# Performance work log

Hardware: AMD Instinct MI355X
Metric: run time of the kernel (lower is better)

The kernel has to match this reference:

```python
import jax, jax.numpy as jnp
import numpy as np

B, S, D = 2, 2048, 1024
H, DH = 16, 64
WINDOW = 256


def setup_inputs() -> dict:
    key = jax.random.key(0)
    ks = jax.random.split(key, 11)
    s = 1.0 / np.sqrt(D)
    return {
        "query": jax.random.normal(ks[0], (B, S, D), jnp.float32),
        "key": jax.random.normal(ks[1], (B, S, D), jnp.float32),
        "value": jax.random.normal(ks[2], (B, S, D), jnp.float32),
        "Wq": jax.random.normal(ks[3], (D, D), jnp.float32) * s,
        "bq": jax.random.normal(ks[4], (D,), jnp.float32) * s,
        "Wk": jax.random.normal(ks[5], (D, D), jnp.float32) * s,
        "bk": jax.random.normal(ks[6], (D,), jnp.float32) * s,
        "Wv": jax.random.normal(ks[7], (D, D), jnp.float32) * s,
        "bv": jax.random.normal(ks[8], (D,), jnp.float32) * s,
        "Wo": jax.random.normal(ks[9], (D, D), jnp.float32) * s,
        "bo": jax.random.normal(ks[10], (D,), jnp.float32) * s,
    }


def reference(query, key, value, Wq, bq, Wk, bk, Wv, bv, Wo, bo):
    scale = DH ** -0.5
    # projections (torch Linear: x @ W.T + b)
    q = query @ Wq.T + bq  # [B,S,D]
    k = key @ Wk.T + bk
    v = value @ Wv.T + bv
    # split heads -> [B,H,S,DH]
    q = q.reshape(B, S, H, DH).transpose(0, 2, 1, 3)
    k = k.reshape(B, S, H, DH).transpose(0, 2, 1, 3)
    v = v.reshape(B, S, H, DH).transpose(0, 2, 1, 3)
    # dense scores with sliding-window causal mask
    attn = jnp.einsum('bhqd,bhkd->bhqk', q, k) * scale  # [B,H,S,S]
    q_idx = jnp.arange(S)[:, None]
    k_idx = jnp.arange(S)[None, :]
    keep = (k_idx <= q_idx) & (k_idx >= q_idx - WINDOW + 1)  # causal & window
    attn = jnp.where(keep[None, None], attn, -jnp.inf)
    attn = jax.nn.softmax(attn, axis=-1)
    # dropout_p=0.0 (eval) -> identity
    out = jnp.einsum('bhqk,bhkd->bhqd', attn, v)  # [B,H,S,DH]
    out = out.transpose(0, 2, 1, 3).reshape(B, S, D)
    return out @ Wo.T + bo
```

## Files before the change

kernel.cpp:

```cpp
#include <hip/hip_runtime.h>
#include <cstdint>
#include <cstddef>

#define B_   2
#define S_   2048
#define D_   1024
#define H_   16
#define DH_  64
#define NROW (B_ * S_)

typedef __bf16  bf16x8 __attribute__((ext_vector_type(8)));
typedef __bf16  bf16x4 __attribute__((ext_vector_type(4)));
typedef float   f32x4  __attribute__((ext_vector_type(4)));

#define MFMA16(a, b, c) __builtin_amdgcn_mfma_f32_16x16x32_bf16((a), (b), (c), 0, 0, 0)

__device__ __forceinline__ void gload_lds16(const void* g, void* l) {
  __builtin_amdgcn_global_load_lds(
      (__attribute__((address_space(1))) void*)(g),
      (__attribute__((address_space(3))) void*)(l), 16, 0, 0);
}

struct CastArgs { const float* src[7]; __bf16* dst[7]; };

__global__ void cast_all(CastArgs a) {
  int b = blockIdx.x, which, idx;
  if (b < 12288) { which = b >> 12; idx = b & 4095; }
  else { b -= 12288; which = 3 + (b >> 10); idx = b & 1023; }
  const int i = idx * 256 + threadIdx.x;
  const float4 v = ((const float4*)a.src[which])[i];
  bf16x4 o;
  o[0] = (__bf16)v.x; o[1] = (__bf16)v.y; o[2] = (__bf16)v.z; o[3] = (__bf16)v.w;
  ((bf16x4*)a.dst[which])[i] = o;
}

struct QKVArgs {
  const __bf16* A[3]; const __bf16* W[3]; const float* bias[3]; __bf16* C[3];
};

__global__ __launch_bounds__(256, 2) void gemm_qkv(QKVArgs args) {
  __shared__ __bf16 As[128 * 32];
  __shared__ __bf16 Bs[128 * 32];
  const int z = blockIdx.z;
  const __bf16* A = args.A[z];
  const __bf16* W = args.W[z];
  const float* bias = args.bias[z];
  __bf16* C = args.C[z];
  const int tid  = threadIdx.x;
  const int lane = tid & 63, wave = tid >> 6;
  const int lo   = lane & 15, quad = lane >> 4;
  const int wr   = wave & 1,  wc   = wave >> 1;
  const int bn   = blockIdx.x, bm = blockIdx.y;
  const __bf16* Ag = A + (size_t)bn * 128 * D_;
  const __bf16* Wg = W + (size_t)bm * 128 * D_;
  const int c0 = tid, c1 = tid + 256;
  const int r0 = c0 >> 2, s0 = (c0 & 3) * 8;
  const int r1 = c1 >> 2, s1 = (c1 & 3) * 8;

  f32x4 acc[4][4] = {};
  for (int k0 = 0; k0 < D_; k0 += 32) {
    __syncthreads();
    gload_lds16(Ag + (size_t)r0 * D_ + k0 + s0, &As[c0 * 8]);
    gload_lds16(Ag + (size_t)r1 * D_ + k0 + s1, &As[c1 * 8]);
    gload_lds16(Wg + (size_t)r0 * D_ + k0 + s0, &Bs[c0 * 8]);
    gload_lds16(Wg + (size_t)r1 * D_ + k0 + s1, &Bs[c1 * 8]);
    __syncthreads();
    bf16x8 af[4], bfr[4];
#pragma unroll
    for (int i = 0; i < 4; i++)
      af[i] = *(const bf16x8*)&As[(wr * 64 + i * 16 + lo) * 32 + quad * 8];
#pragma unroll
    for (int j = 0; j < 4; j++)
      bfr[j] = *(const bf16x8*)&Bs[(wc * 64 + j * 16 + lo) * 32 + quad * 8];
#pragma unroll
    for (int i = 0; i < 4; i++)
#pragma unroll
      for (int j = 0; j < 4; j++)
        acc[i][j] = MFMA16(af[i], bfr[j], acc[i][j]);
  }
  if (z == 2) {
#pragma unroll
    for (int i = 0; i < 4; i++) {
      const int row0 = bn * 128 + wr * 64 + i * 16 + quad * 4;
      const int bb = row0 >> 11, s = row0 & (S_ - 1);
#pragma unroll
      for (int j = 0; j < 4; j++) {
        const int col = bm * 128 + wc * 64 + j * 16 + lo;
        const int hh = col >> 6, dd = col & 63;
        const float bv = bias[col];
        bf16x4 o;
#pragma unroll
        for (int r = 0; r < 4; r++) o[r] = (__bf16)(acc[i][j][r] + bv);
        *(bf16x4*)&C[((size_t)(bb * H_ + hh) * DH_ + dd) * S_ + s] = o;
      }
    }
  } else {
#pragma unroll
    for (int i = 0; i < 4; i++) {
      const int row = bn * 128 + wr * 64 + i * 16 + quad * 4;
#pragma unroll
      for (int j = 0; j < 4; j++) {
        const int col = bm * 128 + wc * 64 + j * 16 + lo;
        const float bv = bias[col];
#pragma unroll
        for (int r = 0; r < 4; r++)
          C[(size_t)(row + r) * D_ + col] = (__bf16)(acc[i][j][r] + bv);
      }
    }
  }
}

__global__ __launch_bounds__(256, 2) void attn_win4(
    const __bf16* __restrict__ Qp, const __bf16* __restrict__ Kp,
    const __bf16* __restrict__ Vt, __bf16* __restrict__ ctx) {
  __shared__ __bf16 smem[20992];
  const int qt = blockIdx.x, h = blockIdx.y, b = blockIdx.z;
  const int q0 = qt * 64;
  const int tid = threadIdx.x, wave = tid >> 6, lane = tid & 63;
  const int lo = lane & 15, quad = lane >> 4;
  const int tmin = (q0 >= 256) ? 0 : ((256 - q0) >> 6);
  const __bf16* Kg = Kp + (size_t)b * S_ * D_ + h * DH_;
  const __bf16* Vg = Vt + (size_t)(b * H_ + h) * DH_ * S_;
  const size_t qbase = ((size_t)b * S_) * D_ + h * DH_;

  const int c0 = tid, c1 = tid + 256;
  const int rA = c0 >> 3, gA = ((c0 & 7) ^ (rA & 7)) * 8;
  const int rB = c1 >> 3, gB = ((c1 & 7) ^ (rB & 7)) * 8;

  auto stageK = [&](int t) {
    const int k0 = q0 - 256 + t * 64;
    const int kb = (t & 1) * 4096;
    gload_lds16(Kg + (size_t)(k0 + rA) * D_ + gA, &smem[kb + c0 * 8]);
    gload_lds16(Kg + (size_t)(k0 + rB) * D_ + gB, &smem[kb + c1 * 8]);
  };
  auto stageV = [&](int t) {
    const int k0 = q0 - 256 + t * 64;
    const int vb = 8192 + (t & 1) * 4096;
    gload_lds16(Vg + (size_t)rA * S_ + k0 + gA, &smem[vb + c0 * 8]);
    gload_lds16(Vg + (size_t)rB * S_ + k0 + gB, &smem[vb + c1 * 8]);
  };

  const int qrow = q0 + wave * 16 + lo;
  const bf16x8 qf0 = *(const bf16x8*)&Qp[qbase + (size_t)qrow * D_ + quad * 8];
  const bf16x8 qf1 = *(const bf16x8*)&Qp[qbase + (size_t)qrow * D_ + 32 + quad * 8];

  stageK(tmin); stageV(tmin);
  if (tmin + 1 <= 4) { stageK(tmin + 1); stageV(tmin + 1); }
  __syncthreads();

  const int g0 = (quad ^ (lo & 7)) * 8;
  const int g1 = ((quad + 4) ^ (lo & 7)) * 8;

  const float scale = 0.125f;
  const int dbase = lo - wave * 16 - quad * 4 - 256;
  const int pw = 16384 + wave * 1152;

  float m_[4] = {-3e38f, -3e38f, -3e38f, -3e38f};
  float l_[4] = {0.f, 0.f, 0.f, 0.f};
  f32x4 oacc[4] = {};

#pragma unroll
  for (int t = 0; t < 5; t++) {
    if (t < tmin) continue;
    const int kb = (t & 1) * 4096, vb = 8192 + (t & 1) * 4096;
    f32x4 sc[4];
#pragma unroll
    for (int kt = 0; kt < 4; kt++) {
      const int kr = kt * 16 + lo;
      const bf16x8 kf0 = *(const bf16x8*)&smem[kb + kr * 64 + g0];
      const bf16x8 kf1 = *(const bf16x8*)&smem[kb + kr * 64 + g1];
      f32x4 c = {0.f, 0.f, 0.f, 0.f};
      c = MFMA16(qf0, kf0, c);
      c = MFMA16(qf1, kf1, c);
      sc[kt] = c;
    }
    float tmax[4] = {-3e38f, -3e38f, -3e38f, -3e38f};
#pragma unroll
    for (int kt = 0; kt < 4; kt++)
#pragma unroll
      for (int r = 0; r < 4; r++) {
        const int delta = dbase + t * 64 + kt * 16 - r;
        const bool keep = (delta <= 0) && (delta > -256);
        const float v = keep ? sc[kt][r] * scale : -3e38f;
        sc[kt][r] = v;
        tmax[r] = fmaxf(tmax[r], v);
      }
#pragma unroll
    for (int r = 0; r < 4; r++)
#pragma unroll
      for (int off = 1; off < 16; off <<= 1)
        tmax[r] = fmaxf(tmax[r], __shfl_xor(tmax[r], off));
    float alpha[4];
#pragma unroll
    for (int r = 0; r < 4; r++) {
      const float mn = fmaxf(m_[r], tmax[r]);
      alpha[r] = __expf(m_[r] - mn);
      m_[r] = mn;
    }
    float rs[4] = {0.f, 0.f, 0.f, 0.f};
#pragma unroll
    for (int kt = 0; kt < 4; kt++)
#pragma unroll
      for (int r = 0; r < 4; r++) {
        const float p = __expf(sc[kt][r] - m_[r]);
        sc[kt][r] = p;
        rs[r] += p;
      }
#pragma unroll
    for (int r = 0; r < 4; r++) {
#pragma unroll
      for (int off = 1; off < 16; off <<= 1)
        rs[r] += __shfl_xor(rs[r], off);
      l_[r] = l_[r] * alpha[r] + rs[r];
    }
#pragma unroll
    for (int ds = 0; ds < 4; ds++)
#pragma unroll
      for (int r = 0; r < 4; r++)
        oacc[ds][r] *= alpha[r];
#pragma unroll
    for (int kt = 0; kt < 4; kt++)
#pragma unroll
      for (int r = 0; r < 4; r++)
        smem[pw + (quad * 4 + r) * 72 + kt * 16 + lo] = (__bf16)sc[kt][r];
    const bf16x8 pf0 = *(const bf16x8*)&smem[pw + lo * 72 + quad * 8];
    const bf16x8 pf1 = *(const bf16x8*)&smem[pw + lo * 72 + 32 + quad * 8];
#pragma unroll
    for (int ds = 0; ds < 4; ds++) {
      const bf16x8 vf0 = *(const bf16x8*)&smem[vb + (ds * 16 + lo) * 64 + g0];
      const bf16x8 vf1 = *(const bf16x8*)&smem[vb + (ds * 16 + lo) * 64 + g1];
      oacc[ds] = MFMA16(pf0, vf0, oacc[ds]);
      oacc[ds] = MFMA16(pf1, vf1, oacc[ds]);
    }
    if (t < 4) {
      __syncthreads();
      if (t + 2 <= 4) { stageK(t + 2); stageV(t + 2); }
    }
  }

#pragma unroll
  for (int ds = 0; ds < 4; ds++)
#pragma unroll
    for (int r = 0; r < 4; r++) {
      const int qg = q0 + wave * 16 + quad * 4 + r;
      ctx[((size_t)b * S_ + qg) * D_ + h * DH_ + ds * 16 + lo] =
          (__bf16)(oacc[ds][r] / l_[r]);
    }
}

__global__ __launch_bounds__(256, 2) void gemm_o(
    const __bf16* __restrict__ A, const __bf16* __restrict__ W,
    const float* __restrict__ bias, float* __restrict__ C) {
  __shared__ __bf16 As[64 * 32];
  __shared__ __bf16 Bs[128 * 32];
  const int tid = threadIdx.x, lane = tid & 63, wave = tid >> 6;
  const int lo = lane & 15, quad = lane >> 4;
  const int wr = wave & 1, wc = wave >> 1;
  const int bn = blockIdx.x, bm = blockIdx.y;
  const __bf16* Ag = A + (size_t)bn * 64 * D_;
  const __bf16* Wg = W + (size_t)bm * 128 * D_;
  const int ra = tid >> 2, sa = (tid & 3) * 8;
  const int cb0 = tid, cb1 = tid + 256;
  const int rb0 = cb0 >> 2, sb0 = (cb0 & 3) * 8;
  const int rb1 = cb1 >> 2, sb1 = (cb1 & 3) * 8;
  f32x4 acc[2][4] = {};
  for (int k0 = 0; k0 < D_; k0 += 32) {
    __syncthreads();
    gload_lds16(Ag + (size_t)ra * D_ + k0 + sa, &As[tid * 8]);
    gload_lds16(Wg + (size_t)rb0 * D_ + k0 + sb0, &Bs[cb0 * 8]);
    gload_lds16(Wg + (size_t)rb1 * D_ + k0 + sb1, &Bs[cb1 * 8]);
    __syncthreads();
    bf16x8 af[2], bfr[4];
#pragma unroll
    for (int i = 0; i < 2; i++)
      af[i] = *(const bf16x8*)&As[(wr * 32 + i * 16 + lo) * 32 + quad * 8];
#pragma unroll
    for (int j = 0; j < 4; j++)
      bfr[j] = *(const bf16x8*)&Bs[(wc * 64 + j * 16 + lo) * 32 + quad * 8];
#pragma unroll
    for (int i = 0; i < 2; i++)
#pragma unroll
      for (int j = 0; j < 4; j++)
        acc[i][j] = MFMA16(af[i], bfr[j], acc[i][j]);
  }
#pragma unroll
  for (int i = 0; i < 2; i++) {
    const int row = bn * 64 + wr * 32 + i * 16 + quad * 4;
#pragma unroll
    for (int j = 0; j < 4; j++) {
      const int col = bm * 128 + wc * 64 + j * 16 + lo;
      const float bv = bias[col];
#pragma unroll
      for (int r = 0; r < 4; r++)
        C[(size_t)(row + r) * D_ + col] = acc[i][j][r] + bv;
    }
  }
}

extern "C" void kernel_launch(void* const* d_in, const int* in_sizes, int n_in,
                              void* d_out, int out_size, void* d_ws, size_t ws_size,
                              hipStream_t stream) {
  (void)in_sizes; (void)n_in; (void)out_size; (void)ws_size;
  const float* q_in = (const float*)d_in[0];
  const float* k_in = (const float*)d_in[1];
  const float* v_in = (const float*)d_in[2];
  const float* Wq   = (const float*)d_in[3];
  const float* bq   = (const float*)d_in[4];
  const float* Wk   = (const float*)d_in[5];
  const float* bk   = (const float*)d_in[6];
  const float* Wv   = (const float*)d_in[7];
  const float* bv   = (const float*)d_in[8];
  const float* Wo   = (const float*)d_in[9];
  const float* bo   = (const float*)d_in[10];

  const size_t XN = (size_t)NROW * D_;
  const size_t WN = (size_t)D_ * D_;
  char* ws = (char*)d_ws;
  __bf16* xq  = (__bf16*)ws; ws += XN * 2;
  __bf16* xk  = (__bf16*)ws; ws += XN * 2;
  __bf16* xv  = (__bf16*)ws; ws += XN * 2;
  __bf16* wqb = (__bf16*)ws; ws += WN * 2;
  __bf16* wkb = (__bf16*)ws; ws += WN * 2;
  __bf16* wvb = (__bf16*)ws; ws += WN * 2;
  __bf16* wob = (__bf16*)ws; ws += WN * 2;
  __bf16* Qp  = (__bf16*)ws; ws += XN * 2;
  __bf16* Kp  = (__bf16*)ws; ws += XN * 2;
  __bf16* Vtp = (__bf16*)ws; ws += XN * 2;
  __bf16* ctx = (__bf16*)ws; ws += XN * 2;

  CastArgs ca;
  ca.src[0] = q_in; ca.src[1] = k_in; ca.src[2] = v_in;
  ca.src[3] = Wq; ca.src[4] = Wk; ca.src[5] = Wv; ca.src[6] = Wo;
  ca.dst[0] = xq; ca.dst[1] = xk; ca.dst[2] = xv;
  ca.dst[3] = wqb; ca.dst[4] = wkb; ca.dst[5] = wvb; ca.dst[6] = wob;
  cast_all<<<16384, 256, 0, stream>>>(ca);

  QKVArgs qa;
  qa.A[0] = xq;  qa.A[1] = xk;  qa.A[2] = xv;
  qa.W[0] = wqb; qa.W[1] = wkb; qa.W[2] = wvb;
  qa.bias[0] = bq; qa.bias[1] = bk; qa.bias[2] = bv;
  qa.C[0] = Qp; qa.C[1] = Kp; qa.C[2] = Vtp;
  gemm_qkv<<<dim3(NROW / 128, D_ / 128, 3), 256, 0, stream>>>(qa);

  attn_win4<<<dim3(S_ / 64, H_, B_), 256, 0, stream>>>(Qp, Kp, Vtp, ctx);

  gemm_o<<<dim3(NROW / 64, D_ / 128), 256, 0, stream>>>(ctx, wob, bo, (float*)d_out);
}
```

Measured before the change: 197.4 us.

## Widen attention query tile to 128 and drop online-softmax max tracking

The sliding-window attention kernel now gives each block 128 query rows, with 32 rows per wave. Each K/V tile staged in LDS is therefore reused across twice as many queries, and the grid is halved. Waves skip K tiles that fall entirely outside their window. The running max, rescale and per-tile shuffle reductions are replaced by a fixed exponent offset, exp(s*scale - 8), and the row sums are reduced once at the end. This saves ALU and shuffle work, but it loses the overflow and underflow protection for large score magnitudes, and the larger LDS footprint with occupancy 3 may limit residency.

Measured after the change: 194.9 us. Within noise of the previous version (-1.3%).

```diff
diff --git a/kernel.cpp b/kernel.cpp
--- a/kernel.cpp
+++ b/kernel.cpp
@@ -110,12 +110,12 @@
   }
 }
 
-__global__ __launch_bounds__(256, 2) void attn_win4(
+__global__ __launch_bounds__(256, 3) void attn_win5(
     const __bf16* __restrict__ Qp, const __bf16* __restrict__ Kp,
     const __bf16* __restrict__ Vt, __bf16* __restrict__ ctx) {
-  __shared__ __bf16 smem[20992];
+  __shared__ __bf16 smem[25600];
   const int qt = blockIdx.x, h = blockIdx.y, b = blockIdx.z;
-  const int q0 = qt * 64;
+  const int q0 = qt * 128;
   const int tid = threadIdx.x, wave = tid >> 6, lane = tid & 63;
   const int lo = lane & 15, quad = lane >> 4;
   const int tmin = (q0 >= 256) ? 0 : ((256 - q0) >> 6);
@@ -140,112 +140,110 @@
     gload_lds16(Vg + (size_t)rB * S_ + k0 + gB, &smem[vb + c1 * 8]);
   };
 
-  const int qrow = q0 + wave * 16 + lo;
-  const bf16x8 qf0 = *(const bf16x8*)&Qp[qbase + (size_t)qrow * D_ + quad * 8];
-  const bf16x8 qf1 = *(const bf16x8*)&Qp[qbase + (size_t)qrow * D_ + 32 + quad * 8];
+  bf16x8 qf[2][2];
+#pragma unroll
+  for (int f = 0; f < 2; f++) {
+    const int qr = q0 + wave * 32 + f * 16 + lo;
+    qf[f][0] = *(const bf16x8*)&Qp[qbase + (size_t)qr * D_ + quad * 8];
+    qf[f][1] = *(const bf16x8*)&Qp[qbase + (size_t)qr * D_ + 32 + quad * 8];
+  }
 
   stageK(tmin); stageV(tmin);
-  if (tmin + 1 <= 4) { stageK(tmin + 1); stageV(tmin + 1); }
+  stageK(tmin + 1); stageV(tmin + 1);
   __syncthreads();
 
   const int g0 = (quad ^ (lo & 7)) * 8;
   const int g1 = ((quad + 4) ^ (lo & 7)) * 8;
 
-  const float scale = 0.125f;
-  const int dbase = lo - wave * 16 - quad * 4 - 256;
-  const int pw = 16384 + wave * 1152;
-
-  float m_[4] = {-3e38f, -3e38f, -3e38f, -3e38f};
-  float l_[4] = {0.f, 0.f, 0.f, 0.f};
-  f32x4 oacc[4] = {};
-
-#pragma unroll
-  for (int t = 0; t < 5; t++) {
+  const int pwb = 16384 + wave * 2304;
+  float rs[2][4] = {};
+  f32x4 oacc[2][4] = {};
+
+#pragma unroll
+  for (int t = 0; t < 6; t++) {
     if (t < tmin) continue;
     const int kb = (t & 1) * 4096, vb = 8192 + (t & 1) * 4096;
-    f32x4 sc[4];
-#pragma unroll
-    for (int kt = 0; kt < 4; kt++) {
-      const int kr = kt * 16 + lo;
-      const bf16x8 kf0 = *(const bf16x8*)&smem[kb + kr * 64 + g0];
-      const bf16x8 kf1 = *(const bf16x8*)&smem[kb + kr * 64 + g1];
-      f32x4 c = {0.f, 0.f, 0.f, 0.f};
-      c = MFMA16(qf0, kf0, c);
-      c = MFMA16(qf1, kf1, c);
-      sc[kt] = c;
-    }
-    float tmax[4] = {-3e38f, -3e38f, -3e38f, -3e38f};
-#pragma unroll
-    for (int kt = 0; kt < 4; kt++)
+    const int kmin = t * 64 - 256;
+    const bool active =
+        (kmin <= wave * 32 + 31) && (kmin + 63 > wave * 32 - 256);
+    if (active) {
+      f32x4 sc[2][4];
+#pragma unroll
+      for (int kt = 0; kt < 4; kt++) {
+        const int kr = kt * 16 + lo;
+        const bf16x8 kf0 = *(const bf16x8*)&smem[kb + kr * 64 + g0];
+        const bf16x8 kf1 = *(const bf16x8*)&smem[kb + kr * 64 + g1];
+#pragma unroll
+        for (int f = 0; f < 2; f++) {
+          f32x4 c = {0.f, 0.f, 0.f, 0.f};
+          c = MFMA16(qf[f][0], kf0, c);
+          c = MFMA16(qf[f][1], kf1, c);
+          sc[f][kt] = c;
+        }
+      }
+#pragma unroll
+      for (int f = 0; f < 2; f++)
+#pragma unroll
+        for (int kt = 0; kt < 4; kt++)
+#pragma unroll
+          for (int r = 0; r < 4; r++) {
+            const int delta =
+                kmin + kt * 16 + lo - (wave * 32 + f * 16 + quad * 4 + r);
+            const bool keep = (delta <= 0) && (delta > -256);
+            const float e = __expf(fmaf(sc[f][kt][r], 0.125f, -8.0f));
+            const float p = keep ? e : 0.0f;
+            sc[f][kt][r] = p;
+            rs[f][r] += p;
+          }
+#pragma unroll
+      for (int f = 0; f < 2; f++)
+#pragma unroll
+        for (int kt = 0; kt < 4; kt++)
+#pragma unroll
+          for (int r = 0; r < 4; r++)
+            smem[pwb + (f * 16 + quad * 4 + r) * 72 + kt * 16 + lo] =
+                (__bf16)sc[f][kt][r];
+      bf16x8 pf[2][2];
+#pragma unroll
+      for (int f = 0; f < 2; f++) {
+        pf[f][0] = *(const bf16x8*)&smem[pwb + (f * 16 + lo) * 72 + quad * 8];
+        pf[f][1] = *(const bf16x8*)&smem[pwb + (f * 16 + lo) * 72 + 32 + quad * 8];
+      }
+#pragma unroll
+      for (int ds = 0; ds < 4; ds++) {
+        const bf16x8 vf0 = *(const bf16x8*)&smem[vb + (ds * 16 + lo) * 64 + g0];
+        const bf16x8 vf1 = *(const bf16x8*)&smem[vb + (ds * 16 + lo) * 64 + g1];
+#pragma unroll
+        for (int f = 0; f < 2; f++) {
+          oacc[f][ds] = MFMA16(pf[f][0], vf0, oacc[f][ds]);
+          oacc[f][ds] = MFMA16(pf[f][1], vf1, oacc[f][ds]);
+        }
+      }
+    }
+    if (t < 5) {
+      __syncthreads();
+      if (t + 2 <= 5) { stageK(t + 2); stageV(t + 2); }
+    }
+  }
+
+#pragma unroll
+  for (int f = 0; f < 2; f++)
+#pragma unroll
+    for (int r = 0; r < 4; r++)
+#pragma unroll
+      for (int off = 1; off < 16; off <<= 1)
+        rs[f][r] += __shfl_xor(rs[f][r], off);
+
+#pragma unroll
+  for (int f = 0; f < 2; f++)
+#pragma unroll
+    for (int ds = 0; ds < 4; ds++)
 #pragma unroll
       for (int r = 0; r < 4; r++) {
-        const int delta = dbase + t * 64 + kt * 16 - r;
-        const bool keep = (delta <= 0) && (delta > -256);
-        const float v = keep ? sc[kt][r] * scale : -3e38f;
-        sc[kt][r] = v;
-        tmax[r] = fmaxf(tmax[r], v);
-      }
-#pragma unroll
-    for (int r = 0; r < 4; r++)
-#pragma unroll
-      for (int off = 1; off < 16; off <<= 1)
-        tmax[r] = fmaxf(tmax[r], __shfl_xor(tmax[r], off));
-    float alpha[4];
-#pragma unroll
-    for (int r = 0; r < 4; r++) {
-      const float mn = fmaxf(m_[r], tmax[r]);
-      alpha[r] = __expf(m_[r] - mn);
-      m_[r] = mn;
-    }
-    float rs[4] = {0.f, 0.f, 0.f, 0.f};
-#pragma unroll
-    for (int kt = 0; kt < 4; kt++)
-#pragma unroll
-      for (int r = 0; r < 4; r++) {
-        const float p = __expf(sc[kt][r] - m_[r]);
-        sc[kt][r] = p;
-        rs[r] += p;
-      }
-#pragma unroll
-    for (int r = 0; r < 4; r++) {
-#pragma unroll
-      for (int off = 1; off < 16; off <<= 1)
-        rs[r] += __shfl_xor(rs[r], off);
-      l_[r] = l_[r] * alpha[r] + rs[r];
-    }
-#pragma unroll
-    for (int ds = 0; ds < 4; ds++)
-#pragma unroll
-      for (int r = 0; r < 4; r++)
-        oacc[ds][r] *= alpha[r];
-#pragma unroll
-    for (int kt = 0; kt < 4; kt++)
-#pragma unroll
-      for (int r = 0; r < 4; r++)
-        smem[pw + (quad * 4 + r) * 72 + kt * 16 + lo] = (__bf16)sc[kt][r];
-    const bf16x8 pf0 = *(const bf16x8*)&smem[pw + lo * 72 + quad * 8];
-    const bf16x8 pf1 = *(const bf16x8*)&smem[pw + lo * 72 + 32 + quad * 8];
-#pragma unroll
-    for (int ds = 0; ds < 4; ds++) {
-      const bf16x8 vf0 = *(const bf16x8*)&smem[vb + (ds * 16 + lo) * 64 + g0];
-      const bf16x8 vf1 = *(const bf16x8*)&smem[vb + (ds * 16 + lo) * 64 + g1];
-      oacc[ds] = MFMA16(pf0, vf0, oacc[ds]);
-      oacc[ds] = MFMA16(pf1, vf1, oacc[ds]);
-    }
-    if (t < 4) {
-      __syncthreads();
-      if (t + 2 <= 4) { stageK(t + 2); stageV(t + 2); }
-    }
-  }
-
-#pragma unroll
-  for (int ds = 0; ds < 4; ds++)
-#pragma unroll
-    for (int r = 0; r < 4; r++) {
-      const int qg = q0 + wave * 16 + quad * 4 + r;
-      ctx[((size_t)b * S_ + qg) * D_ + h * DH_ + ds * 16 + lo] =
-          (__bf16)(oacc[ds][r] / l_[r]);
-    }
+        const int qg = q0 + wave * 32 + f * 16 + quad * 4 + r;
+        ctx[((size_t)b * S_ + qg) * D_ + h * DH_ + ds * 16 + lo] =
+            (__bf16)(oacc[f][ds][r] / rs[f][r]);
+      }
 }
 
 __global__ __launch_bounds__(256, 2) void gemm_o(
@@ -342,7 +340,7 @@
   qa.C[0] = Qp; qa.C[1] = Kp; qa.C[2] = Vtp;
   gemm_qkv<<<dim3(NROW / 128, D_ / 128, 3), 256, 0, stream>>>(qa);
 
-  attn_win4<<<dim3(S_ / 64, H_, B_), 256, 0, stream>>>(Qp, Kp, Vtp, ctx);
+  attn_win5<<<dim3(S_ / 128, H_, B_), 256, 0, stream>>>(Qp, Kp, Vtp, ctx);
 
   gemm_o<<<dim3(NROW / 64, D_ / 128), 256, 0, stream>>>(ctx, wob, bo, (float*)d_out);
 }
```
